# Optimization experiments

Measured on AMD Instinct MI355X. Metric: run time of the kernel, lower is better.

## Reference

```python
import jax, jax.numpy as jnp
import numpy as np
from jax import lax

T, B = 128, 256
I, H = 512, 1024
V, O = 128, 64


def setup_inputs() -> dict:
    key = jax.random.key(0)
    ks = jax.random.split(key, 8)
    s_ih = 1.0 / np.sqrt(H)
    return {
        "input": jax.random.randint(ks[0], (T, B), 0, V, dtype=jnp.int64),
        "h0": jnp.zeros((1, B, H), jnp.float32),
        "c0": jnp.zeros((1, B, H), jnp.float32),
        "emb": jax.random.normal(ks[1], (V, I), jnp.float32),
        "w_ih": jax.random.uniform(ks[2], (4 * H, I), jnp.float32, -s_ih, s_ih),
        "w_hh": jax.random.uniform(ks[3], (4 * H, H), jnp.float32, -s_ih, s_ih),
        "b_ih": jax.random.uniform(ks[4], (4 * H,), jnp.float32, -s_ih, s_ih),
        "b_hh": jax.random.uniform(ks[5], (4 * H,), jnp.float32, -s_ih, s_ih),
        "w_out": jax.random.uniform(ks[6], (O, H), jnp.float32, -s_ih, s_ih),
        "b_out": jax.random.uniform(ks[7], (O,), jnp.float32, -s_ih, s_ih),
    }


def reference(input, h0, c0, emb, w_ih, w_hh, b_ih, b_hh, w_out, b_out):
    # Embedding lookup: [T, B] -> [T, B, I]
    x = emb[input]
    b = b_ih + b_hh  # fuse the two bias adds

    def step(carry, xt):
        h, c = carry  # [B, H] each
        gates = xt @ w_ih.T + h @ w_hh.T + b  # [B, 4H]
        i, f, g, o = jnp.split(gates, 4, axis=-1)  # torch gate order: i,f,g,o
        i = jax.nn.sigmoid(i)
        f = jax.nn.sigmoid(f)
        g = jnp.tanh(g)
        o = jax.nn.sigmoid(o)
        c_new = f * c + i * g
        h_new = o * jnp.tanh(c_new)
        return (h_new, c_new), h_new

    (h_last, _), _ = lax.scan(step, (h0[0], c0[0]), x)
    # out_layer(lstm_out[-1].unsqueeze(0))[-1] == last hidden through linear head
    return h_last @ w_out.T + b_out  # [B, O]
```

## Files before the change

### kernel.cpp

```cpp
#include <hip/hip_runtime.h>

typedef __attribute__((ext_vector_type(4)))  int int4v;
typedef __attribute__((ext_vector_type(16))) int i32x16;

union B16 { int4v v; signed char c[16]; };

__device__ __forceinline__ float rcp_(float x){ return __builtin_amdgcn_rcpf(x); }
__device__ __forceinline__ float sigm(float x){ return rcp_(1.f + __expf(-x)); }
__device__ __forceinline__ float tanh_(float x){
  float e = __expf(-2.f * fabsf(x));
  float r = (1.f - e) * rcp_(1.f + e);
  return copysignf(r, x);
}
__device__ __forceinline__ void h_limbs(float h, int& a1, int& a0){
  float f1 = floorf(h * 128.f);
  f1 = fminf(fmaxf(f1, -128.f), 127.f);
  float r = fmaf(h, 32768.f, f1 * -256.f) - 128.f;
  float f0 = fminf(rintf(r), 127.f);
  a1 = (int)f1; a0 = (int)f0;
}

__device__ __forceinline__ void issue_l128_cc(const void* p, int4v& d){
  asm volatile("global_load_dwordx4 %0, %1, off sc0 sc1" : "=&v"(d) : "v"(p) : "memory");
}

__global__ __launch_bounds__(256) void prep_kernel(
    const float* __restrict__ emb, const float* __restrict__ w_ih,
    const float* __restrict__ b_ih, const float* __restrict__ b_hh,
    const float* __restrict__ h0, float* __restrict__ G_in,
    char* __restrict__ a1buf, char* __restrict__ a0buf)
{
  __shared__ __align__(16) float wt[16 * 512];
  const int tid = threadIdx.x;
  const int colbase = blockIdx.x << 4;
  #pragma unroll
  for (int i = 0; i < 8; ++i){
    int f = tid + (i << 8);
    int r = f >> 7, q = (f & 127) << 2;
    *(float4*)&wt[(r << 9) + q] = *(const float4*)&w_ih[((size_t)(colbase + r) << 9) + q];
  }
  __syncthreads();
  const int v_ = tid & 127, ch = tid >> 7;
  float acc[8] = {0,0,0,0,0,0,0,0};
  const float* ep = emb + ((size_t)v_ << 9);
  for (int kq = 0; kq < 128; ++kq){
    float4 e = *(const float4*)(ep + (kq << 2));
    #pragma unroll
    for (int c = 0; c < 8; ++c){
      float4 w = *(const float4*)&wt[(((ch << 3) + c) << 9) + (kq << 2)];
      acc[c] += e.x * w.x + e.y * w.y + e.z * w.z + e.w * w.w;
    }
  }
  const int col0 = colbase + (ch << 3);
  #pragma unroll
  for (int c = 0; c < 8; ++c) acc[c] += b_ih[col0 + c] + b_hh[col0 + c];
  float* gp = &G_in[((size_t)v_ << 12) + col0];
  float4 r0 = {acc[0], acc[1], acc[2], acc[3]};
  float4 r1 = {acc[4], acc[5], acc[6], acc[7]};
  *(float4*)gp = r0;
  *(float4*)(gp + 4) = r1;

  int g0 = (blockIdx.x << 10) + (tid << 2);
  float4 hv = *(const float4*)&h0[g0];
  int a1x,a0x,a1y,a0y,a1z,a0z,a1w,a0w;
  h_limbs(hv.x, a1x, a0x); h_limbs(hv.y, a1y, a0y);
  h_limbs(hv.z, a1z, a0z); h_limbs(hv.w, a1w, a0w);
  unsigned u1 = (unsigned)(a1x & 255) | ((unsigned)(a1y & 255) << 8)
              | ((unsigned)(a1z & 255) << 16) | ((unsigned)(a1w & 255) << 24);
  unsigned u0 = (unsigned)(a0x & 255) | ((unsigned)(a0y & 255) << 8)
              | ((unsigned)(a0z & 255) << 16) | ((unsigned)(a0w & 255) << 24);
  ((unsigned*)a1buf)[g0 >> 2] = u1;
  ((unsigned*)a0buf)[g0 >> 2] = u0;
}

__global__ __launch_bounds__(512, 1) void lstm_kernel(
    const int* __restrict__ input, const float* __restrict__ c0,
    const float* __restrict__ w_hh, const float* __restrict__ w_out,
    const float* __restrict__ b_out, const float* __restrict__ G_in,
    char* __restrict__ a1base, char* __restrict__ a0base,
    unsigned* __restrict__ flags, float* __restrict__ out)
{
  const int tid  = threadIdx.x;
  const int lane = tid & 63;
  const int wid  = tid >> 6;
  const int gate = wid & 3;
  const int half = wid >> 2;
  const int bg   = blockIdx.x >> 5;
  const int cg   = blockIdx.x & 31;
  const int row  = tid & 31;
  const int grp  = tid >> 5;

  __shared__ __align__(16) unsigned long long sA1[4096];
  __shared__ __align__(16) unsigned long long sA0[4096];
  __shared__ __align__(16) float sGa[32 * 132];
  __shared__ __align__(16) float sGb[32 * 132];
  __shared__ float sKc2[2][128];

  int4v b1f[16], b0f[16];
  {
    const float* wrow = w_hh + (size_t)(gate * 1024 + cg * 32 + (lane & 31)) * 1024;
    const int kb0 = (lane >> 5) << 4;
    float csum = 0.f;
    #pragma unroll
    for (int ksl = 0; ksl < 16; ++ksl){
      const int gks = (ksl & 7) + ((ksl >> 3) << 4) + (half << 3);
      B16 v1, v0;
      #pragma unroll
      for (int q = 0; q < 4; ++q){
        float4 w4 = *(const float4*)&wrow[gks * 32 + kb0 + (q << 2)];
        float wa[4] = {w4.x, w4.y, w4.z, w4.w};
        #pragma unroll
        for (int j = 0; j < 4; ++j){
          float w = wa[j];
          csum += w;
          float s1 = rintf(w * 2048.f);
          float s0 = fminf(rintf(fmaf(w, 524288.f, s1 * -256.f)), 127.f);
          v1.c[(q << 2) + j] = (signed char)(int)s1;
          v0.c[(q << 2) + j] = (signed char)(int)s0;
        }
      }
      b1f[ksl] = v1.v; b0f[ksl] = v0.v;
    }
    csum += __shfl_xor(csum, 32, 64);
    if (lane < 32) sKc2[half][(gate << 5) + lane] = csum * 0.00390625f;
  }

  const int bl = (tid >> 3) & 31;
  const int u4 = (tid & 7) << 2;
  const int b  = (bg << 5) + bl;
  float4 cr = {0,0,0,0};
  if (tid < 256) cr = *(const float4*)&c0[((size_t)b << 10) + (cg << 5) + u4];
  unsigned* slots = &flags[bg * 32];
  unsigned* myslot = &flags[bg * 32 + cg];
  const size_t rbase = (size_t)((bg << 5) + row) << 10;

  #pragma unroll 1
  for (int t = 0; t < 128; ++t){
    const char* s1b = a1base + (size_t)(t & 1) * 262144;
    const char* s0b = a0base + (size_t)(t & 1) * 262144;
    char* d1b = a1base + (size_t)((t + 1) & 1) * 262144;
    char* d0b = a0base + (size_t)((t + 1) & 1) * 262144;
    const unsigned target = (unsigned)t;

    float4 q0 = {0,0,0,0}, q1 = {0,0,0,0}, q2 = {0,0,0,0}, q3 = {0,0,0,0};
    if (tid < 256){
      int iv = input[t * 256 + b];
      const float* gp = G_in + ((size_t)iv << 12) + (cg << 5) + u4;
      q0 = *(const float4*)(gp);
      q1 = *(const float4*)(gp + 1024);
      q2 = *(const float4*)(gp + 2048);
      q3 = *(const float4*)(gp + 3072);
    }

    if (wid == 0 && target){
      int guard = 0;
      for (;;){
        unsigned v = (lane < 32)
          ? __hip_atomic_load(&slots[lane], __ATOMIC_RELAXED, __HIP_MEMORY_SCOPE_AGENT)
          : 0xFFFFFFFFu;
        if (__ballot(lane >= 16 || v >= target) == ~0ull) break;
        if (++guard > (1 << 20)) break;
      }
    }
    __syncthreads();

    int4v gv1[4], gv0[4];
    #pragma unroll
    for (int i = 0; i < 2; ++i){
      size_t off = rbase + ((size_t)(grp + (i << 4)) << 4);
      issue_l128_cc(s1b + off, gv1[i]);
      issue_l128_cc(s0b + off, gv0[i]);
    }

    if (wid == 0 && target){
      int guard = 0;
      for (;;){
        unsigned v = (lane < 32)
          ? __hip_atomic_load(&slots[lane], __ATOMIC_RELAXED, __HIP_MEMORY_SCOPE_AGENT)
          : 0xFFFFFFFFu;
        if (__ballot(v >= target) == ~0ull) break;
        if (++guard > (1 << 20)) break;
      }
    }
    __syncthreads();

    #pragma unroll
    for (int i = 2; i < 4; ++i){
      size_t off = rbase + ((size_t)(grp + (i << 4)) << 4);
      issue_l128_cc(s1b + off, gv1[i]);
      issue_l128_cc(s0b + off, gv0[i]);
    }

    i32x16 acc_hi = {}, acc_m1 = {}, acc_m2 = {};
    const int4v* A1 = (const int4v*)sA1;
    const int4v* A0 = (const int4v*)sA0;
    #pragma unroll
    for (int c = 0; c < 4; ++c){
      if      (c == 0) asm volatile("s_waitcnt vmcnt(6)" ::: "memory");
      else if (c == 1) asm volatile("s_waitcnt vmcnt(4)" ::: "memory");
      else if (c == 2) asm volatile("s_waitcnt vmcnt(2)" ::: "memory");
      else             asm volatile("s_waitcnt vmcnt(0)" ::: "memory");
      __builtin_amdgcn_sched_barrier(0);
      {
        const int m = grp + (c << 4);
        const int lidx = ((((m >> 1) << 6) + ((m & 1) << 5) + row)) << 1;
        *(int4v*)&sA1[lidx] = gv1[c];
        *(int4v*)&sA0[lidx] = gv0[c];
      }
      asm volatile("s_waitcnt lgkmcnt(0)" ::: "memory");
      __builtin_amdgcn_sched_barrier(0);
      __builtin_amdgcn_s_barrier();
      __builtin_amdgcn_sched_barrier(0);
      if (half == (c & 1)){
        const int ksl0 = (c >> 1) << 3;
        #pragma unroll
        for (int k8 = 0; k8 < 8; ++k8){
          const int ks  = (c << 3) + k8;
          const int ksl = ksl0 + k8;
          int4v af1 = A1[(ks << 6) + lane];
          acc_hi = __builtin_amdgcn_mfma_i32_32x32x32_i8(af1, b1f[ksl], acc_hi, 0, 0, 0);
          acc_m1 = __builtin_amdgcn_mfma_i32_32x32x32_i8(af1, b0f[ksl], acc_m1, 0, 0, 0);
          int4v af0 = A0[(ks << 6) + lane];
          acc_m2 = __builtin_amdgcn_mfma_i32_32x32x32_i8(af0, b1f[ksl], acc_m2, 0, 0, 0);
        }
      }
    }

    {
      float* sGh = half ? sGb : sGa;
      const int col = (gate << 5) + (lane & 31);
      const int rb  = (lane >> 5) << 2;
      #pragma unroll
      for (int r = 0; r < 16; ++r){
        int rrow = (r & 3) + ((r >> 2) << 3) + rb;
        sGh[rrow * 132 + col] = 3.814697265625e-06f     * (float)acc_hi[r]
                              + 1.4901161193847656e-08f * (float)(acc_m1[r] + acc_m2[r]);
      }
    }
    __syncthreads();

    if (tid < 256){
      float4 kIa = *(const float4*)&sKc2[0][ 0 + u4], kIb = *(const float4*)&sKc2[1][ 0 + u4];
      float4 kFa = *(const float4*)&sKc2[0][32 + u4], kFb = *(const float4*)&sKc2[1][32 + u4];
      float4 kGa = *(const float4*)&sKc2[0][64 + u4], kGb = *(const float4*)&sKc2[1][64 + u4];
      float4 kOa = *(const float4*)&sKc2[0][96 + u4], kOb = *(const float4*)&sKc2[1][96 + u4];
      float4 gIa = *(const float4*)&sGa[bl * 132 +  0 + u4], gIb = *(const float4*)&sGb[bl * 132 +  0 + u4];
      float4 gFa = *(const float4*)&sGa[bl * 132 + 32 + u4], gFb = *(const float4*)&sGb[bl * 132 + 32 + u4];
      float4 gGa = *(const float4*)&sGa[bl * 132 + 64 + u4], gGb = *(const float4*)&sGb[bl * 132 + 64 + u4];
      float4 gOa = *(const float4*)&sGa[bl * 132 + 96 + u4], gOb = *(const float4*)&sGb[bl * 132 + 96 + u4];
      float4 gI = {gIa.x+gIb.x, gIa.y+gIb.y, gIa.z+gIb.z, gIa.w+gIb.w};
      float4 gF = {gFa.x+gFb.x, gFa.y+gFb.y, gFa.z+gFb.z, gFa.w+gFb.w};
      float4 gG = {gGa.x+gGb.x, gGa.y+gGb.y, gGa.z+gGb.z, gGa.w+gGb.w};
      float4 gO = {gOa.x+gOb.x, gOa.y+gOb.y, gOa.z+gOb.z, gOa.w+gOb.w};
      float4 kI = {kIa.x+kIb.x, kIa.y+kIb.y, kIa.z+kIb.z, kIa.w+kIb.w};
      float4 kF = {kFa.x+kFb.x, kFa.y+kFb.y, kFa.z+kFb.z, kFa.w+kFb.w};
      float4 kG = {kGa.x+kGb.x, kGa.y+kGb.y, kGa.z+kGb.z, kGa.w+kGb.w};
      float4 kO = {kOa.x+kOb.x, kOa.y+kOb.y, kOa.z+kOb.z, kOa.w+kOb.w};
      int a1x,a0x,a1y,a0y,a1z,a0z,a1w,a0w;
      { float I=sigm(gI.x+q0.x+kI.x), F=sigm(gF.x+q1.x+kF.x), G=tanh_(gG.x+q2.x+kG.x), O=sigm(gO.x+q3.x+kO.x);
        float Cn=F*cr.x+I*G; cr.x=Cn; h_limbs(O*tanh_(Cn), a1x, a0x); }
      { float I=sigm(gI.y+q0.y+kI.y), F=sigm(gF.y+q1.y+kF.y), G=tanh_(gG.y+q2.y+kG.y), O=sigm(gO.y+q3.y+kO.y);
        float Cn=F*cr.y+I*G; cr.y=Cn; h_limbs(O*tanh_(Cn), a1y, a0y); }
      { float I=sigm(gI.z+q0.z+kI.z), F=sigm(gF.z+q1.z+kF.z), G=tanh_(gG.z+q2.z+kG.z), O=sigm(gO.z+q3.z+kO.z);
        float Cn=F*cr.z+I*G; cr.z=Cn; h_limbs(O*tanh_(Cn), a1z, a0z); }
      { float I=sigm(gI.w+q0.w+kI.w), F=sigm(gF.w+q1.w+kF.w), G=tanh_(gG.w+q2.w+kG.w), O=sigm(gO.w+q3.w+kO.w);
        float Cn=F*cr.w+I*G; cr.w=Cn; h_limbs(O*tanh_(Cn), a1w, a0w); }
      unsigned u1 = (unsigned)(a1x & 255) | ((unsigned)(a1y & 255) << 8)
                  | ((unsigned)(a1z & 255) << 16) | ((unsigned)(a1w & 255) << 24);
      unsigned u0 = (unsigned)(a0x & 255) | ((unsigned)(a0y & 255) << 8)
                  | ((unsigned)(a0z & 255) << 16) | ((unsigned)(a0w & 255) << 24);
      size_t eidx = (((size_t)b << 10) + (cg << 5) + u4) >> 2;
      __hip_atomic_store((unsigned*)d1b + eidx, u1, __ATOMIC_RELAXED, __HIP_MEMORY_SCOPE_AGENT);
      __hip_atomic_store((unsigned*)d0b + eidx, u0, __ATOMIC_RELAXED, __HIP_MEMORY_SCOPE_AGENT);
    }
    __syncthreads();
    if (tid == 0)
      __hip_atomic_store(myslot, (unsigned)(t + 1), __ATOMIC_RELAXED, __HIP_MEMORY_SCOPE_AGENT);
  }

  if (wid == 0){
    int guard = 0;
    for (;;){
      unsigned v = (lane < 32)
        ? __hip_atomic_load(&slots[lane], __ATOMIC_RELAXED, __HIP_MEMORY_SCOPE_AGENT)
        : 0xFFFFFFFFu;
      if (__ballot(v >= 128u) == ~0ull) break;
      if (++guard > (1 << 20)) break;
    }
  }
  __syncthreads();
  if (tid < 256){
    const unsigned* h1p = (const unsigned*)a1base;
    const unsigned* h0p = (const unsigned*)a0base;
    const int ksl = tid & 7;
    const int o0 = cg << 1;
    float s0 = 0.f, s1 = 0.f;
    const float* w0p = w_out + ((size_t)o0 << 10);
    const float* w1p = w0p + 1024;
    for (int k = ksl * 128; k < ksl * 128 + 128; k += 4){
      size_t idx = (((size_t)b << 10) + k) >> 2;
      unsigned v1 = __hip_atomic_load(h1p + idx, __ATOMIC_RELAXED, __HIP_MEMORY_SCOPE_AGENT);
      unsigned v0 = __hip_atomic_load(h0p + idx, __ATOMIC_RELAXED, __HIP_MEMORY_SCOPE_AGENT);
      float4 w0 = *(const float4*)(w0p + k);
      float4 w1 = *(const float4*)(w1p + k);
      float hh[4];
      #pragma unroll
      for (int j = 0; j < 4; ++j){
        int A1j = (int)(signed char)((v1 >> (8 * j)) & 255);
        int A0j = (int)(signed char)((v0 >> (8 * j)) & 255);
        hh[j] = (float)(A1j * 256 + A0j + 128) * 3.0517578125e-05f;
      }
      s0 += hh[0]*w0.x + hh[1]*w0.y + hh[2]*w0.z + hh[3]*w0.w;
      s1 += hh[0]*w1.x + hh[1]*w1.y + hh[2]*w1.z + hh[3]*w1.w;
    }
    sGa[bl * 16 + (ksl << 1)]     = s0;
    sGa[bl * 16 + (ksl << 1) + 1] = s1;
  }
  __syncthreads();
  if (tid < 64){
    int bl2 = tid >> 1, ol = tid & 1;
    float s = b_out[(cg << 1) + ol];
    #pragma unroll
    for (int q = 0; q < 8; ++q) s += sGa[bl2 * 16 + (q << 1) + ol];
    out[((size_t)((bg << 5) + bl2) << 6) + (cg << 1) + ol] = s;
  }
}

extern "C" void kernel_launch(void* const* d_in, const int* in_sizes, int n_in,
                              void* d_out, int out_size, void* d_ws, size_t ws_size,
                              hipStream_t stream){
  (void)in_sizes; (void)n_in; (void)out_size; (void)ws_size;
  const int* input   = (const int*)d_in[0];
  const float* h0    = (const float*)d_in[1];
  const float* c0    = (const float*)d_in[2];
  const float* emb   = (const float*)d_in[3];
  const float* w_ih  = (const float*)d_in[4];
  const float* w_hh  = (const float*)d_in[5];
  const float* b_ih  = (const float*)d_in[6];
  const float* b_hh  = (const float*)d_in[7];
  const float* w_out = (const float*)d_in[8];
  const float* b_out = (const float*)d_in[9];
  float* out = (float*)d_out;

  char* ws = (char*)d_ws;
  float* G_in   = (float*)ws;
  char* a1buf   = ws + (2u << 20);
  char* a0buf   = ws + (2u << 20) + (512u << 10);
  unsigned* flags = (unsigned*)(ws + (3u << 20));

  hipMemsetAsync(flags, 0, 4096, stream);
  prep_kernel<<<dim3(256), dim3(256), 0, stream>>>(emb, w_ih, b_ih, b_hh, h0, G_in, a1buf, a0buf);

  void* args[] = {(void*)&input, (void*)&c0, (void*)&w_hh, (void*)&w_out, (void*)&b_out,
                  (void*)&G_in, (void*)&a1buf, (void*)&a0buf, (void*)&flags, (void*)&out};
  if (hipLaunchCooperativeKernel((void*)lstm_kernel, dim3(256), dim3(512), args, 0, stream)
      != hipSuccess){
    lstm_kernel<<<dim3(256), dim3(512), 0, stream>>>(input, c0, w_hh, w_out, b_out,
                                                     G_in, a1buf, a0buf, flags, out);
  }
}
```

Measured before the change: 943.9 us.

## Split workgroup into independent halves with LDS half-barriers and per-half K slices

Each half of the workgroup (4 waves) now owns a contiguous K range of h, loads only its own slice from global memory, and synchronises with a custom LDS atomic counter barrier instead of full __syncthreads. The wait on producer flags is split so each half waits only on the 16 column groups it consumes, letting the halves proceed independently. The pointwise LSTM update is spread over all 512 threads with two units each, using a lane shuffle to pack the output bytes. The cost is spin-waiting on LDS atomics, and the halves still meet at the full barrier before the gate reduction.

```diff
diff --git a/kernel.cpp b/kernel.cpp
--- a/kernel.cpp
+++ b/kernel.cpp
@@ -88,13 +88,16 @@
   const int bg   = blockIdx.x >> 5;
   const int cg   = blockIdx.x & 31;
   const int row  = tid & 31;
-  const int grp  = tid >> 5;
+  const int grp8 = (tid >> 5) & 7;
 
   __shared__ __align__(16) unsigned long long sA1[4096];
   __shared__ __align__(16) unsigned long long sA0[4096];
   __shared__ __align__(16) float sGa[32 * 132];
   __shared__ __align__(16) float sGb[32 * 132];
   __shared__ float sKc2[2][128];
+  __shared__ unsigned hbar[2];
+
+  if (tid < 2) hbar[tid] = 0;
 
   int4v b1f[16], b0f[16];
   {
@@ -102,37 +105,48 @@
     const int kb0 = (lane >> 5) << 4;
     float csum = 0.f;
     #pragma unroll
-    for (int ksl = 0; ksl < 16; ++ksl){
-      const int gks = (ksl & 7) + ((ksl >> 3) << 4) + (half << 3);
+    for (int j = 0; j < 16; ++j){
+      const int gks = (half << 4) + j;
       B16 v1, v0;
       #pragma unroll
       for (int q = 0; q < 4; ++q){
         float4 w4 = *(const float4*)&wrow[gks * 32 + kb0 + (q << 2)];
         float wa[4] = {w4.x, w4.y, w4.z, w4.w};
         #pragma unroll
-        for (int j = 0; j < 4; ++j){
-          float w = wa[j];
+        for (int jj = 0; jj < 4; ++jj){
+          float w = wa[jj];
           csum += w;
           float s1 = rintf(w * 2048.f);
           float s0 = fminf(rintf(fmaf(w, 524288.f, s1 * -256.f)), 127.f);
-          v1.c[(q << 2) + j] = (signed char)(int)s1;
-          v0.c[(q << 2) + j] = (signed char)(int)s0;
+          v1.c[(q << 2) + jj] = (signed char)(int)s1;
+          v0.c[(q << 2) + jj] = (signed char)(int)s0;
         }
       }
-      b1f[ksl] = v1.v; b0f[ksl] = v0.v;
+      b1f[j] = v1.v; b0f[j] = v0.v;
     }
     csum += __shfl_xor(csum, 32, 64);
     if (lane < 32) sKc2[half][(gate << 5) + lane] = csum * 0.00390625f;
   }
-
-  const int bl = (tid >> 3) & 31;
-  const int u4 = (tid & 7) << 2;
+  __syncthreads();
+
+  const int bl = tid >> 4;
+  const int u2 = (tid & 15) << 1;
   const int b  = (bg << 5) + bl;
-  float4 cr = {0,0,0,0};
-  if (tid < 256) cr = *(const float4*)&c0[((size_t)b << 10) + (cg << 5) + u4];
+  float2 cr = *(const float2*)&c0[((size_t)b << 10) + (cg << 5) + u2];
   unsigned* slots = &flags[bg * 32];
   unsigned* myslot = &flags[bg * 32 + cg];
   const size_t rbase = (size_t)((bg << 5) + row) << 10;
+  unsigned hgen = 0;
+
+  #define HALFBAR() do { \
+    asm volatile("s_waitcnt lgkmcnt(0)" ::: "memory"); \
+    if (lane == 0) __hip_atomic_fetch_add(&hbar[half], 1u, __ATOMIC_RELAXED, __HIP_MEMORY_SCOPE_WORKGROUP); \
+    ++hgen; \
+    int g_ = 0; \
+    while (__hip_atomic_load(&hbar[half], __ATOMIC_RELAXED, __HIP_MEMORY_SCOPE_WORKGROUP) < 4u*hgen) { \
+      if (++g_ > (1 << 20)) break; } \
+    __builtin_amdgcn_sched_barrier(0); \
+  } while(0)
 
   #pragma unroll 1
   for (int t = 0; t < 128; ++t){
@@ -142,51 +156,41 @@
     char* d0b = a0base + (size_t)((t + 1) & 1) * 262144;
     const unsigned target = (unsigned)t;
 
-    float4 q0 = {0,0,0,0}, q1 = {0,0,0,0}, q2 = {0,0,0,0}, q3 = {0,0,0,0};
-    if (tid < 256){
-      int iv = input[t * 256 + b];
-      const float* gp = G_in + ((size_t)iv << 12) + (cg << 5) + u4;
-      q0 = *(const float4*)(gp);
-      q1 = *(const float4*)(gp + 1024);
-      q2 = *(const float4*)(gp + 2048);
-      q3 = *(const float4*)(gp + 3072);
-    }
-
-    if (wid == 0 && target){
-      int guard = 0;
-      for (;;){
-        unsigned v = (lane < 32)
-          ? __hip_atomic_load(&slots[lane], __ATOMIC_RELAXED, __HIP_MEMORY_SCOPE_AGENT)
-          : 0xFFFFFFFFu;
-        if (__ballot(lane >= 16 || v >= target) == ~0ull) break;
-        if (++guard > (1 << 20)) break;
-      }
-    }
-    __syncthreads();
+    int iv = input[t * 256 + b];
+    const float* gp = G_in + ((size_t)iv << 12) + (cg << 5) + u2;
+    float2 q0 = *(const float2*)(gp);
+    float2 q1 = *(const float2*)(gp + 1024);
+    float2 q2 = *(const float2*)(gp + 2048);
+    float2 q3 = *(const float2*)(gp + 3072);
+
+    if (target){
+      if (wid == 0){
+        int guard = 0;
+        for (;;){
+          unsigned v = (lane < 32)
+            ? __hip_atomic_load(&slots[lane], __ATOMIC_RELAXED, __HIP_MEMORY_SCOPE_AGENT)
+            : 0xFFFFFFFFu;
+          if (__ballot(lane >= 16 || v >= target) == ~0ull) break;
+          if (++guard > (1 << 20)) break;
+        }
+      } else if (wid == 4){
+        int guard = 0;
+        for (;;){
+          unsigned v = (lane < 32)
+            ? __hip_atomic_load(&slots[lane], __ATOMIC_RELAXED, __HIP_MEMORY_SCOPE_AGENT)
+            : 0xFFFFFFFFu;
+          if (__ballot(lane < 16 || lane >= 32 || v >= target) == ~0ull) break;
+          if (++guard > (1 << 20)) break;
+        }
+      }
+    }
+    HALFBAR();
 
     int4v gv1[4], gv0[4];
     #pragma unroll
-    for (int i = 0; i < 2; ++i){
-      size_t off = rbase + ((size_t)(grp + (i << 4)) << 4);
-      issue_l128_cc(s1b + off, gv1[i]);
-      issue_l128_cc(s0b + off, gv0[i]);
-    }
-
-    if (wid == 0 && target){
-      int guard = 0;
-      for (;;){
-        unsigned v = (lane < 32)
-          ? __hip_atomic_load(&slots[lane], __ATOMIC_RELAXED, __HIP_MEMORY_SCOPE_AGENT)
-          : 0xFFFFFFFFu;
-        if (__ballot(v >= target) == ~0ull) break;
-        if (++guard > (1 << 20)) break;
-      }
-    }
-    __syncthreads();
-
-    #pragma unroll
-    for (int i = 2; i < 4; ++i){
-      size_t off = rbase + ((size_t)(grp + (i << 4)) << 4);
+    for (int i = 0; i < 4; ++i){
+      const int m = (half << 5) + grp8 + (i << 3);
+      size_t off = rbase + ((size_t)m << 4);
       issue_l128_cc(s1b + off, gv1[i]);
       issue_l128_cc(s0b + off, gv0[i]);
     }
@@ -194,36 +198,45 @@
     i32x16 acc_hi = {}, acc_m1 = {}, acc_m2 = {};
     const int4v* A1 = (const int4v*)sA1;
     const int4v* A0 = (const int4v*)sA0;
-    #pragma unroll
-    for (int c = 0; c < 4; ++c){
-      if      (c == 0) asm volatile("s_waitcnt vmcnt(6)" ::: "memory");
-      else if (c == 1) asm volatile("s_waitcnt vmcnt(4)" ::: "memory");
-      else if (c == 2) asm volatile("s_waitcnt vmcnt(2)" ::: "memory");
-      else             asm volatile("s_waitcnt vmcnt(0)" ::: "memory");
-      __builtin_amdgcn_sched_barrier(0);
-      {
-        const int m = grp + (c << 4);
-        const int lidx = ((((m >> 1) << 6) + ((m & 1) << 5) + row)) << 1;
-        *(int4v*)&sA1[lidx] = gv1[c];
-        *(int4v*)&sA0[lidx] = gv0[c];
-      }
-      asm volatile("s_waitcnt lgkmcnt(0)" ::: "memory");
-      __builtin_amdgcn_sched_barrier(0);
-      __builtin_amdgcn_s_barrier();
-      __builtin_amdgcn_sched_barrier(0);
-      if (half == (c & 1)){
-        const int ksl0 = (c >> 1) << 3;
-        #pragma unroll
-        for (int k8 = 0; k8 < 8; ++k8){
-          const int ks  = (c << 3) + k8;
-          const int ksl = ksl0 + k8;
-          int4v af1 = A1[(ks << 6) + lane];
-          acc_hi = __builtin_amdgcn_mfma_i32_32x32x32_i8(af1, b1f[ksl], acc_hi, 0, 0, 0);
-          acc_m1 = __builtin_amdgcn_mfma_i32_32x32x32_i8(af1, b0f[ksl], acc_m1, 0, 0, 0);
-          int4v af0 = A0[(ks << 6) + lane];
-          acc_m2 = __builtin_amdgcn_mfma_i32_32x32x32_i8(af0, b1f[ksl], acc_m2, 0, 0, 0);
-        }
-      }
+
+    asm volatile("s_waitcnt vmcnt(4)" ::: "memory");
+    __builtin_amdgcn_sched_barrier(0);
+    #pragma unroll
+    for (int i = 0; i < 2; ++i){
+      const int m = (half << 5) + grp8 + (i << 3);
+      const int lidx = ((((m >> 1) << 6) + ((m & 1) << 5) + row)) << 1;
+      *(int4v*)&sA1[lidx] = gv1[i];
+      *(int4v*)&sA0[lidx] = gv0[i];
+    }
+    HALFBAR();
+    #pragma unroll
+    for (int j = 0; j < 8; ++j){
+      const int ks = (half << 4) + j;
+      int4v af1 = A1[(ks << 6) + lane];
+      acc_hi = __builtin_amdgcn_mfma_i32_32x32x32_i8(af1, b1f[j], acc_hi, 0, 0, 0);
+      acc_m1 = __builtin_amdgcn_mfma_i32_32x32x32_i8(af1, b0f[j], acc_m1, 0, 0, 0);
+      int4v af0 = A0[(ks << 6) + lane];
+      acc_m2 = __builtin_amdgcn_mfma_i32_32x32x32_i8(af0, b1f[j], acc_m2, 0, 0, 0);
+    }
+
+    asm volatile("s_waitcnt vmcnt(0)" ::: "memory");
+    __builtin_amdgcn_sched_barrier(0);
+    #pragma unroll
+    for (int i = 2; i < 4; ++i){
+      const int m = (half << 5) + grp8 + (i << 3);
+      const int lidx = ((((m >> 1) << 6) + ((m & 1) << 5) + row)) << 1;
+      *(int4v*)&sA1[lidx] = gv1[i];
+      *(int4v*)&sA0[lidx] = gv0[i];
+    }
+    HALFBAR();
+    #pragma unroll
+    for (int j = 8; j < 16; ++j){
+      const int ks = (half << 4) + j;
+      int4v af1 = A1[(ks << 6) + lane];
+      acc_hi = __builtin_amdgcn_mfma_i32_32x32x32_i8(af1, b1f[j], acc_hi, 0, 0, 0);
+      acc_m1 = __builtin_amdgcn_mfma_i32_32x32x32_i8(af1, b0f[j], acc_m1, 0, 0, 0);
+      int4v af0 = A0[(ks << 6) + lane];
+      acc_m2 = __builtin_amdgcn_mfma_i32_32x32x32_i8(af0, b1f[j], acc_m2, 0, 0, 0);
     }
 
     {
@@ -239,39 +252,33 @@
     }
     __syncthreads();
 
-    if (tid < 256){
-      float4 kIa = *(const float4*)&sKc2[0][ 0 + u4], kIb = *(const float4*)&sKc2[1][ 0 + u4];
-      float4 kFa = *(const float4*)&sKc2[0][32 + u4], kFb = *(const float4*)&sKc2[1][32 + u4];
-      float4 kGa = *(const float4*)&sKc2[0][64 + u4], kGb = *(const float4*)&sKc2[1][64 + u4];
-      float4 kOa = *(const float4*)&sKc2[0][96 + u4], kOb = *(const float4*)&sKc2[1][96 + u4];
-      float4 gIa = *(const float4*)&sGa[bl * 132 +  0 + u4], gIb = *(const float4*)&sGb[bl * 132 +  0 + u4];
-      float4 gFa = *(const float4*)&sGa[bl * 132 + 32 + u4], gFb = *(const float4*)&sGb[bl * 132 + 32 + u4];
-      float4 gGa = *(const float4*)&sGa[bl * 132 + 64 + u4], gGb = *(const float4*)&sGb[bl * 132 + 64 + u4];
-      float4 gOa = *(const float4*)&sGa[bl * 132 + 96 + u4], gOb = *(const float4*)&sGb[bl * 132 + 96 + u4];
-      float4 gI = {gIa.x+gIb.x, gIa.y+gIb.y, gIa.z+gIb.z, gIa.w+gIb.w};
-      float4 gF = {gFa.x+gFb.x, gFa.y+gFb.y, gFa.z+gFb.z, gFa.w+gFb.w};
-      float4 gG = {gGa.x+gGb.x, gGa.y+gGb.y, gGa.z+gGb.z, gGa.w+gGb.w};
-      float4 gO = {gOa.x+gOb.x, gOa.y+gOb.y, gOa.z+gOb.z, gOa.w+gOb.w};
-      float4 kI = {kIa.x+kIb.x, kIa.y+kIb.y, kIa.z+kIb.z, kIa.w+kIb.w};
-      float4 kF = {kFa.x+kFb.x, kFa.y+kFb.y, kFa.z+kFb.z, kFa.w+kFb.w};
-      float4 kG = {kGa.x+kGb.x, kGa.y+kGb.y, kGa.z+kGb.z, kGa.w+kGb.w};
-      float4 kO = {kOa.x+kOb.x, kOa.y+kOb.y, kOa.z+kOb.z, kOa.w+kOb.w};
-      int a1x,a0x,a1y,a0y,a1z,a0z,a1w,a0w;
+    {
+      float2 kI = {sKc2[0][ 0 + u2] + sKc2[1][ 0 + u2], sKc2[0][ 1 + u2] + sKc2[1][ 1 + u2]};
+      float2 kF = {sKc2[0][32 + u2] + sKc2[1][32 + u2], sKc2[0][33 + u2] + sKc2[1][33 + u2]};
+      float2 kG = {sKc2[0][64 + u2] + sKc2[1][64 + u2], sKc2[0][65 + u2] + sKc2[1][65 + u2]};
+      float2 kO = {sKc2[0][96 + u2] + sKc2[1][96 + u2], sKc2[0][97 + u2] + sKc2[1][97 + u2]};
+      const float* ga = &sGa[bl * 132];
+      const float* gb = &sGb[bl * 132];
+      float2 gI = {ga[ 0 + u2] + gb[ 0 + u2], ga[ 1 + u2] + gb[ 1 + u2]};
+      float2 gF = {ga[32 + u2] + gb[32 + u2], ga[33 + u2] + gb[33 + u2]};
+      float2 gG = {ga[64 + u2] + gb[64 + u2], ga[65 + u2] + gb[65 + u2]};
+      float2 gO = {ga[96 + u2] + gb[96 + u2], ga[97 + u2] + gb[97 + u2]};
+      int a1a,a0a,a1b,a0b;
       { float I=sigm(gI.x+q0.x+kI.x), F=sigm(gF.x+q1.x+kF.x), G=tanh_(gG.x+q2.x+kG.x), O=sigm(gO.x+q3.x+kO.x);
-        float Cn=F*cr.x+I*G; cr.x=Cn; h_limbs(O*tanh_(Cn), a1x, a0x); }
+        float Cn=F*cr.x+I*G; cr.x=Cn; h_limbs(O*tanh_(Cn), a1a, a0a); }
       { float I=sigm(gI.y+q0.y+kI.y), F=sigm(gF.y+q1.y+kF.y), G=tanh_(gG.y+q2.y+kG.y), O=sigm(gO.y+q3.y+kO.y);
-        float Cn=F*cr.y+I*G; cr.y=Cn; h_limbs(O*tanh_(Cn), a1y, a0y); }
-      { float I=sigm(gI.z+q0.z+kI.z), F=sigm(gF.z+q1.z+kF.z), G=tanh_(gG.z+q2.z+kG.z), O=sigm(gO.z+q3.z+kO.z);
-        float Cn=F*cr.z+I*G; cr.z=Cn; h_limbs(O*tanh_(Cn), a1z, a0z); }
-      { float I=sigm(gI.w+q0.w+kI.w), F=sigm(gF.w+q1.w+kF.w), G=tanh_(gG.w+q2.w+kG.w), O=sigm(gO.w+q3.w+kO.w);
-        float Cn=F*cr.w+I*G; cr.w=Cn; h_limbs(O*tanh_(Cn), a1w, a0w); }
-      unsigned u1 = (unsigned)(a1x & 255) | ((unsigned)(a1y & 255) << 8)
-                  | ((unsigned)(a1z & 255) << 16) | ((unsigned)(a1w & 255) << 24);
-      unsigned u0 = (unsigned)(a0x & 255) | ((unsigned)(a0y & 255) << 8)
-                  | ((unsigned)(a0z & 255) << 16) | ((unsigned)(a0w & 255) << 24);
-      size_t eidx = (((size_t)b << 10) + (cg << 5) + u4) >> 2;
-      __hip_atomic_store((unsigned*)d1b + eidx, u1, __ATOMIC_RELAXED, __HIP_MEMORY_SCOPE_AGENT);
-      __hip_atomic_store((unsigned*)d0b + eidx, u0, __ATOMIC_RELAXED, __HIP_MEMORY_SCOPE_AGENT);
+        float Cn=F*cr.y+I*G; cr.y=Cn; h_limbs(O*tanh_(Cn), a1b, a0b); }
+      unsigned m1 = (unsigned)(a1a & 255) | ((unsigned)(a1b & 255) << 8);
+      unsigned m0 = (unsigned)(a0a & 255) | ((unsigned)(a0b & 255) << 8);
+      unsigned p1 = __shfl_xor(m1, 1, 64);
+      unsigned p0 = __shfl_xor(m0, 1, 64);
+      if (!(tid & 1)){
+        unsigned w1 = m1 | (p1 << 16);
+        unsigned w0 = m0 | (p0 << 16);
+        size_t eidx = (((size_t)b << 10) + (cg << 5) + u2) >> 2;
+        __hip_atomic_store((unsigned*)d1b + eidx, w1, __ATOMIC_RELAXED, __HIP_MEMORY_SCOPE_AGENT);
+        __hip_atomic_store((unsigned*)d0b + eidx, w0, __ATOMIC_RELAXED, __HIP_MEMORY_SCOPE_AGENT);
+      }
     }
     __syncthreads();
     if (tid == 0)
@@ -292,13 +299,15 @@
   if (tid < 256){
     const unsigned* h1p = (const unsigned*)a1base;
     const unsigned* h0p = (const unsigned*)a0base;
+    const int hbl = (tid >> 3) & 31;
+    const int hb  = (bg << 5) + hbl;
     const int ksl = tid & 7;
     const int o0 = cg << 1;
     float s0 = 0.f, s1 = 0.f;
     const float* w0p = w_out + ((size_t)o0 << 10);
     const float* w1p = w0p + 1024;
     for (int k = ksl * 128; k < ksl * 128 + 128; k += 4){
-      size_t idx = (((size_t)b << 10) + k) >> 2;
+      size_t idx = (((size_t)hb << 10) + k) >> 2;
       unsigned v1 = __hip_atomic_load(h1p + idx, __ATOMIC_RELAXED, __HIP_MEMORY_SCOPE_AGENT);
       unsigned v0 = __hip_atomic_load(h0p + idx, __ATOMIC_RELAXED, __HIP_MEMORY_SCOPE_AGENT);
       float4 w0 = *(const float4*)(w0p + k);
@@ -313,8 +322,8 @@
       s0 += hh[0]*w0.x + hh[1]*w0.y + hh[2]*w0.z + hh[3]*w0.w;
       s1 += hh[0]*w1.x + hh[1]*w1.y + hh[2]*w1.z + hh[3]*w1.w;
     }
-    sGa[bl * 16 + (ksl << 1)]     = s0;
-    sGa[bl * 16 + (ksl << 1) + 1] = s1;
+    sGa[hbl * 16 + (ksl << 1)]     = s0;
+    sGa[hbl * 16 + (ksl << 1) + 1] = s1;
   }
   __syncthreads();
   if (tid < 64){
@@ -324,6 +333,7 @@
     for (int q = 0; q < 8; ++q) s += sGa[bl2 * 16 + (q << 1) + ol];
     out[((size_t)((bg << 5) + bl2) << 6) + (cg << 1) + ol] = s;
   }
+  #undef HALFBAR
 }
 
 extern "C" void kernel_launch(void* const* d_in, const int* in_sizes, int n_in,
```

Measured after the change: 979.7 us. 1.04x slower.
